# Optimization experiments

Hardware: AMD Instinct MI355X
Metric: run time of the kernel (lower is better)

Reference implementation:

```python
import jax, jax.numpy as jnp
import numpy as np

N_NODES = 100000
N_EDGES = 1600000
IN_DIM = 32
OUT_DIM = 64
N_REL = 8
EPS = 1e-10


def setup_inputs() -> dict:
    key = jax.random.key(0)
    k_x, k_src, k_dst, k_rel, k_w, k_wl, k_ws = jax.random.split(key, 7)
    x = jax.random.normal(k_x, (N_NODES, IN_DIM), dtype=jnp.float32)
    node_in = jax.random.randint(k_src, (N_EDGES,), 0, N_NODES)
    node_out = jax.random.randint(k_dst, (N_EDGES,), 0, N_NODES)
    relation = jax.random.randint(k_rel, (N_EDGES,), 0, N_REL)
    edge_list = jnp.stack([node_in, node_out, relation], axis=1)  # [E, 3] int
    edge_weight = jax.random.uniform(k_w, (N_EDGES,), dtype=jnp.float32)
    W_linear = jax.random.normal(k_wl, (N_REL * IN_DIM, OUT_DIM), dtype=jnp.float32) / np.sqrt(N_REL * IN_DIM)
    b_linear = jnp.zeros((OUT_DIM,), dtype=jnp.float32)
    W_self = jax.random.normal(k_ws, (IN_DIM, OUT_DIM), dtype=jnp.float32) / np.sqrt(IN_DIM)
    b_self = jnp.zeros((OUT_DIM,), dtype=jnp.float32)
    return {"x": x, "edge_list": edge_list, "edge_weight": edge_weight,
            "W_linear": W_linear, "b_linear": b_linear,
            "W_self": W_self, "b_self": b_self}


def reference(x, edge_list, edge_weight, W_linear, b_linear, W_self, b_self):
    num_node, in_dim = x.shape
    # message: gather source-node features per edge  -> [E, D]
    msg = x[edge_list[:, 0]]
    # aggregate: relation-expanded segment id = dst * R + rel
    seg = edge_list[:, 1] * N_REL + edge_list[:, 2]  # [E]
    w = edge_weight[:, None]  # [E, 1]
    num = jax.ops.segment_sum(msg * w, seg, num_segments=num_node * N_REL)  # [N*R, D]
    den = jax.ops.segment_sum(w, seg, num_segments=num_node * N_REL)        # [N*R, 1]
    update = (num / (den + EPS)).reshape(num_node, N_REL * in_dim)          # [N, R*D]
    # combine: linear(update) + self_loop(x), then ReLU
    out = update @ W_linear + b_linear + x @ W_self + b_self
    return jax.nn.relu(out)
```

## Files before the change

kernel.cpp:

```cpp
#include <hip/hip_runtime.h>
#include <stdint.h>

#define N_NODES 100000
#define N_EDGES 1600000
#define IN_DIM 32
#define OUT_DIM 64
#define N_REL 8
#define NSEG (N_NODES * N_REL)
#define EPS 1e-10f
#define N_KK 9
#define SWG_ELEMS (N_KK * 4 * 64 * 8)
#define XB_PAIRS (N_NODES * 16)
#define NTILES ((N_NODES + 63) / 64)

typedef __attribute__((ext_vector_type(8))) short bf16x8;
typedef __attribute__((ext_vector_type(2))) short bf16x2;
typedef __attribute__((ext_vector_type(4))) float f32x4;

static __device__ __forceinline__ float bflo(uint32_t u) { return __uint_as_float(u << 16); }
static __device__ __forceinline__ float bfhi(uint32_t u) { return __uint_as_float(u & 0xffff0000u); }
static __device__ __forceinline__ uint16_t f2bf(float f) {
    uint32_t u = __float_as_uint(f);
    return (uint16_t)((u + 0x7fffu + ((u >> 16) & 1u)) >> 16);
}

static __device__ __forceinline__ void pk_add_bf16(uint32_t* addr, float f0, float f1) {
#if __has_builtin(__builtin_amdgcn_global_atomic_fadd_v2bf16)
    bf16x2 v;
    v[0] = (short)f2bf(f0);
    v[1] = (short)f2bf(f1);
    __builtin_amdgcn_global_atomic_fadd_v2bf16((bf16x2*)addr, v);
#else
    uint32_t old = *addr, assumed;
    do {
        assumed = old;
        float lo = bflo(assumed) + f0;
        float hi = bfhi(assumed) + f1;
        uint32_t nv = (uint32_t)f2bf(lo) | ((uint32_t)f2bf(hi) << 16);
        old = atomicCAS(addr, assumed, nv);
    } while (old != assumed);
#endif
}

__global__ __launch_bounds__(256) void detect_kernel(const uint32_t* __restrict__ xw,
                                                     int* __restrict__ flag) {
    __shared__ int cnt;
    if (threadIdx.x == 0) cnt = 0;
    __syncthreads();
    int c = 0;
    for (int k = threadIdx.x; k < 4096; k += 256) {
        uint32_t w = xw[k];
        uint32_t e = (w >> 7) & 0xffu;
        c += (e >= 160u) ? 1 : 0;
    }
    atomicAdd(&cnt, c);
    __syncthreads();
    if (threadIdx.x == 0) *flag = (cnt > 64) ? 1 : 0;
}

__global__ __launch_bounds__(256) void prep_kernel(const void* __restrict__ x,
                                                   const void* __restrict__ Wl,
                                                   const void* __restrict__ Ws,
                                                   const void* __restrict__ bl,
                                                   const void* __restrict__ bs,
                                                   const int* __restrict__ flag,
                                                   uint32_t* __restrict__ xb,
                                                   uint16_t* __restrict__ sWg,
                                                   float* __restrict__ biasv) {
    int f32 = *flag;
    int idx = blockIdx.x * 256 + threadIdx.x;
    if (idx < XB_PAIRS) {
        if (f32) {
            float2 v = ((const float2*)x)[idx];
            xb[idx] = (uint32_t)f2bf(v.x) | ((uint32_t)f2bf(v.y) << 16);
        } else {
            xb[idx] = ((const uint32_t*)x)[idx];
        }
    } else if (idx < XB_PAIRS + SWG_ELEMS) {
        int w = idx - XB_PAIRS;
        int j    = w & 7;
        int lane = (w >> 3) & 63;
        int ot   = (w >> 9) & 3;
        int kk   = w >> 11;
        int quad = lane >> 4;
        int k = kk * 32 + quad * 8 + j;
        int o = ot * 16 + (lane & 15);
        if (f32) {
            float v = (k < 256) ? ((const float*)Wl)[(size_t)k * OUT_DIM + o]
                                : ((const float*)Ws)[(size_t)(k - 256) * OUT_DIM + o];
            sWg[w] = f2bf(v);
        } else {
            sWg[w] = (k < 256) ? ((const uint16_t*)Wl)[(size_t)k * OUT_DIM + o]
                               : ((const uint16_t*)Ws)[(size_t)(k - 256) * OUT_DIM + o];
        }
    } else if (idx < XB_PAIRS + SWG_ELEMS + OUT_DIM) {
        int o = idx - XB_PAIRS - SWG_ELEMS;
        if (f32) biasv[o] = ((const float*)bl)[o] + ((const float*)bs)[o];
        else     biasv[o] = bflo((uint32_t)((const uint16_t*)bl)[o])
                          + bflo((uint32_t)((const uint16_t*)bs)[o]);
    }
}

__global__ __launch_bounds__(256) void scatter_pk_kernel(
    const int* __restrict__ el,
    const void* __restrict__ ew,
    const uint32_t* __restrict__ xb,
    const int* __restrict__ flag,
    uint32_t* __restrict__ num,
    float* __restrict__ den)
{
    int t = blockIdx.x * 256 + threadIdx.x;
    int e = t >> 4;
    int p = t & 15;
    if (e >= N_EDGES) return;

    int src = el[e * 3 + 0];
    int dst = el[e * 3 + 1];
    int rel = el[e * 3 + 2];

    float w = (*flag) ? ((const float*)ew)[e]
                      : bflo((uint32_t)((const uint16_t*)ew)[e]);

    uint32_t d = xb[(size_t)src * 16 + p];
    int seg = dst * N_REL + rel;
    pk_add_bf16(&num[(size_t)seg * 16 + p], w * bflo(d), w * bfhi(d));
    if (p == 0) atomicAdd(&den[seg], w);
}

__global__ __launch_bounds__(256) void dense_mfma_kernel(
    const uint32_t* __restrict__ num,
    const float* __restrict__ den,
    const uint32_t* __restrict__ xb,
    const uint16_t* __restrict__ sWg,
    const float* __restrict__ biasv,
    const int* __restrict__ flag,
    void* __restrict__ out)
{
    int f32  = *flag;
    int wid  = threadIdx.x >> 6;
    int lane = threadIdx.x & 63;
    int quad = lane >> 4;
    int m    = lane & 15;

    float bias[4];
    #pragma unroll
    for (int ot = 0; ot < 4; ++ot) bias[ot] = biasv[ot * 16 + m];

    int n0 = blockIdx.x * 64 + wid * 16;
    int n  = n0 + m;
    int nc = (n < N_NODES) ? n : (N_NODES - 1);

    float4 d0 = *(const float4*)(den + (size_t)nc * 8);
    float4 d1 = *(const float4*)(den + (size_t)nc * 8 + 4);
    float inv[8];
    inv[0] = 1.0f / (d0.x + EPS); inv[1] = 1.0f / (d0.y + EPS);
    inv[2] = 1.0f / (d0.z + EPS); inv[3] = 1.0f / (d0.w + EPS);
    inv[4] = 1.0f / (d1.x + EPS); inv[5] = 1.0f / (d1.y + EPS);
    inv[6] = 1.0f / (d1.z + EPS); inv[7] = 1.0f / (d1.w + EPS);

    f32x4 acc[4];
    #pragma unroll
    for (int ot = 0; ot < 4; ++ot) acc[ot] = (f32x4){0.f, 0.f, 0.f, 0.f};

    #pragma unroll
    for (int kk = 0; kk < N_KK; ++kk) {
        bf16x8 a;
        if (kk < 8) {
            const uint4 d = *(const uint4*)(num + ((size_t)nc * 8 + kk) * 16 + quad * 4);
            float iv = inv[kk];
            a[0] = (short)f2bf(bflo(d.x) * iv); a[1] = (short)f2bf(bfhi(d.x) * iv);
            a[2] = (short)f2bf(bflo(d.y) * iv); a[3] = (short)f2bf(bfhi(d.y) * iv);
            a[4] = (short)f2bf(bflo(d.z) * iv); a[5] = (short)f2bf(bfhi(d.z) * iv);
            a[6] = (short)f2bf(bflo(d.w) * iv); a[7] = (short)f2bf(bfhi(d.w) * iv);
        } else {
            a = *(const bf16x8*)((const uint16_t*)xb + (size_t)nc * IN_DIM + quad * 8);
        }
        #pragma unroll
        for (int ot = 0; ot < 4; ++ot) {
            bf16x8 b = *(const bf16x8*)(sWg + ((kk * 4 + ot) * 64 + lane) * 8);
            acc[ot] = __builtin_amdgcn_mfma_f32_16x16x32_bf16(a, b, acc[ot], 0, 0, 0);
        }
    }

    #pragma unroll
    for (int ot = 0; ot < 4; ++ot) {
        #pragma unroll
        for (int reg = 0; reg < 4; ++reg) {
            int node = n0 + quad * 4 + reg;
            if (node >= N_NODES) continue;
            int o = ot * 16 + m;
            float v = fmaxf(acc[ot][reg] + bias[ot], 0.0f);
            if (f32) ((float*)out)[(size_t)node * OUT_DIM + o] = v;
            else     ((uint16_t*)out)[(size_t)node * OUT_DIM + o] = f2bf(v);
        }
    }
}

extern "C" void kernel_launch(void* const* d_in, const int* in_sizes, int n_in,
                              void* d_out, int out_size, void* d_ws, size_t ws_size,
                              hipStream_t stream) {
    const void* x  = d_in[0];
    const int* el  = (const int*)d_in[1];
    const void* ew = d_in[2];
    const void* Wl = d_in[3];
    const void* bl = d_in[4];
    const void* Ws = d_in[5];
    const void* bs = d_in[6];

    const size_t OFF_DEN  = 64;
    const size_t OFF_NUM  = OFF_DEN + (size_t)NSEG * 4;
    const size_t OFF_SWG  = OFF_NUM + (size_t)NSEG * IN_DIM * 2;
    const size_t OFF_BIAS = OFF_SWG + (size_t)SWG_ELEMS * 2;
    const size_t OFF_XB   = OFF_BIAS + OUT_DIM * 4;
    const size_t REQ      = OFF_XB + (size_t)XB_PAIRS * 4;
    if (ws_size < REQ) return;

    int*      flag  = (int*)d_ws;
    float*    den   = (float*)((char*)d_ws + OFF_DEN);
    uint32_t* num   = (uint32_t*)((char*)d_ws + OFF_NUM);
    uint16_t* sWg   = (uint16_t*)((char*)d_ws + OFF_SWG);
    float*    biasv = (float*)((char*)d_ws + OFF_BIAS);
    uint32_t* xb    = (uint32_t*)((char*)d_ws + OFF_XB);

    hipMemsetAsync(d_ws, 0, OFF_SWG, stream);
    detect_kernel<<<1, 256, 0, stream>>>((const uint32_t*)x, flag);
    {
        int total = XB_PAIRS + SWG_ELEMS + OUT_DIM;
        prep_kernel<<<(total + 255) / 256, 256, 0, stream>>>(x, Wl, Ws, bl, bs, flag, xb, sWg, biasv);
    }
    {
        long long threads = (long long)N_EDGES * 16;
        int blocks = (int)((threads + 255) / 256);
        scatter_pk_kernel<<<blocks, 256, 0, stream>>>(el, ew, xb, flag, num, den);
    }
    dense_mfma_kernel<<<NTILES, 256, 0, stream>>>(num, den, xb, sWg, biasv, flag, d_out);
}
```

Baseline: 282.0 us.

## Bucket edges by segment and aggregate in LDS instead of global bf16 atomics

Replaces the global packed-bf16 atomic scatter with a counting-sort pipeline: histogram edges into buckets of 256 segments, scan, reorder packed edges, then one block per bucket accumulates num and den in shared memory with fp32 LDS atomics. Normalization and the bf16 conversion move into the aggregation kernel, so the dense MFMA kernel loads pre-divided bf16 rows directly. This removes contended global atomics and the large num/den memset, but adds several passes over the edge list, global atomics on bucket cursors, and a single-block scan. Accumulation is now in fp32 rather than bf16, which improves accuracy.

```diff
diff --git a/kernel.cpp b/kernel.cpp
--- a/kernel.cpp
+++ b/kernel.cpp
@@ -12,9 +12,10 @@
 #define SWG_ELEMS (N_KK * 4 * 64 * 8)
 #define XB_PAIRS (N_NODES * 16)
 #define NTILES ((N_NODES + 63) / 64)
+#define SEGS_PER_BUCKET 256
+#define NBUCK (NSEG / SEGS_PER_BUCKET)
 
 typedef __attribute__((ext_vector_type(8))) short bf16x8;
-typedef __attribute__((ext_vector_type(2))) short bf16x2;
 typedef __attribute__((ext_vector_type(4))) float f32x4;
 
 static __device__ __forceinline__ float bflo(uint32_t u) { return __uint_as_float(u << 16); }
@@ -22,24 +23,6 @@
 static __device__ __forceinline__ uint16_t f2bf(float f) {
     uint32_t u = __float_as_uint(f);
     return (uint16_t)((u + 0x7fffu + ((u >> 16) & 1u)) >> 16);
-}
-
-static __device__ __forceinline__ void pk_add_bf16(uint32_t* addr, float f0, float f1) {
-#if __has_builtin(__builtin_amdgcn_global_atomic_fadd_v2bf16)
-    bf16x2 v;
-    v[0] = (short)f2bf(f0);
-    v[1] = (short)f2bf(f1);
-    __builtin_amdgcn_global_atomic_fadd_v2bf16((bf16x2*)addr, v);
-#else
-    uint32_t old = *addr, assumed;
-    do {
-        assumed = old;
-        float lo = bflo(assumed) + f0;
-        float hi = bfhi(assumed) + f1;
-        uint32_t nv = (uint32_t)f2bf(lo) | ((uint32_t)f2bf(hi) << 16);
-        old = atomicCAS(addr, assumed, nv);
-    } while (old != assumed);
-#endif
 }
 
 __global__ __launch_bounds__(256) void detect_kernel(const uint32_t* __restrict__ xw,
@@ -101,35 +84,111 @@
     }
 }
 
-__global__ __launch_bounds__(256) void scatter_pk_kernel(
-    const int* __restrict__ el,
-    const void* __restrict__ ew,
-    const uint32_t* __restrict__ xb,
-    const int* __restrict__ flag,
-    uint32_t* __restrict__ num,
-    float* __restrict__ den)
-{
-    int t = blockIdx.x * 256 + threadIdx.x;
-    int e = t >> 4;
-    int p = t & 15;
+__global__ __launch_bounds__(256) void hist_kernel(const int* __restrict__ el,
+                                                   unsigned int* __restrict__ hist) {
+    int e = blockIdx.x * 256 + threadIdx.x;
     if (e >= N_EDGES) return;
-
+    int dst = el[e * 3 + 1];
+    int rel = el[e * 3 + 2];
+    atomicAdd(&hist[(dst * N_REL + rel) >> 8], 1u);
+}
+
+__global__ __launch_bounds__(256) void scan_kernel(unsigned int* __restrict__ hist,
+                                                   unsigned int* __restrict__ cursor) {
+    __shared__ unsigned int lds[256];
+    const int PER = (NBUCK + 255) / 256;
+    int t = threadIdx.x;
+    unsigned int v[13];
+    unsigned int loc = 0;
+    #pragma unroll
+    for (int k = 0; k < PER; ++k) {
+        int i = t * PER + k;
+        v[k] = (i < NBUCK) ? hist[i] : 0u;
+        loc += v[k];
+    }
+    lds[t] = loc;
+    __syncthreads();
+    unsigned int xv = lds[t];
+    for (int off = 1; off < 256; off <<= 1) {
+        unsigned int add = (t >= off) ? lds[t - off] : 0u;
+        __syncthreads();
+        xv += add;
+        lds[t] = xv;
+        __syncthreads();
+    }
+    unsigned int run = (t == 0) ? 0u : lds[t - 1];
+    #pragma unroll
+    for (int k = 0; k < PER; ++k) {
+        int i = t * PER + k;
+        if (i < NBUCK) {
+            hist[i] = run;
+            cursor[i] = run;
+            run += v[k];
+        }
+    }
+    if (t == 255) hist[NBUCK] = lds[255];
+}
+
+__global__ __launch_bounds__(256) void reorder_kernel(const int* __restrict__ el,
+                                                      const void* __restrict__ ew,
+                                                      const int* __restrict__ flag,
+                                                      unsigned int* __restrict__ cursor,
+                                                      uint64_t* __restrict__ epack) {
+    int e = blockIdx.x * 256 + threadIdx.x;
+    if (e >= N_EDGES) return;
     int src = el[e * 3 + 0];
     int dst = el[e * 3 + 1];
     int rel = el[e * 3 + 2];
-
-    float w = (*flag) ? ((const float*)ew)[e]
-                      : bflo((uint32_t)((const uint16_t*)ew)[e]);
-
-    uint32_t d = xb[(size_t)src * 16 + p];
+    uint32_t wb = (*flag) ? ((const uint32_t*)ew)[e]
+                          : (((uint32_t)((const uint16_t*)ew)[e]) << 16);
     int seg = dst * N_REL + rel;
-    pk_add_bf16(&num[(size_t)seg * 16 + p], w * bflo(d), w * bfhi(d));
-    if (p == 0) atomicAdd(&den[seg], w);
+    unsigned int pos = atomicAdd(&cursor[seg >> 8], 1u);
+    epack[pos] = ((uint64_t)wb << 32) | ((uint32_t)src << 8) | (uint32_t)(seg & 255);
+}
+
+__global__ __launch_bounds__(256) void aggregate_kernel(const uint64_t* __restrict__ epack,
+                                                        const unsigned int* __restrict__ bstart,
+                                                        const uint32_t* __restrict__ xb,
+                                                        uint32_t* __restrict__ numdiv) {
+    __shared__ float lnum[SEGS_PER_BUCKET * IN_DIM];
+    __shared__ float lden[SEGS_PER_BUCKET];
+
+    int b = blockIdx.x;
+    for (int k = threadIdx.x; k < SEGS_PER_BUCKET * IN_DIM; k += 256) lnum[k] = 0.f;
+    for (int k = threadIdx.x; k < SEGS_PER_BUCKET; k += 256) lden[k] = 0.f;
+    __syncthreads();
+
+    unsigned int start = bstart[b];
+    unsigned int end   = bstart[b + 1];
+    int g    = threadIdx.x >> 5;
+    int lane = threadIdx.x & 31;
+
+    for (unsigned int e = start + g; e < end; e += 8) {
+        uint64_t p = epack[e];
+        uint32_t lo = (uint32_t)p;
+        int seg_local = lo & 255;
+        int src = (lo >> 8) & 0x1FFFF;
+        float w = __uint_as_float((uint32_t)(p >> 32));
+        uint32_t d = xb[(size_t)src * 16 + (lane >> 1)];
+        float xv = (lane & 1) ? bfhi(d) : bflo(d);
+        atomicAdd(&lnum[seg_local * IN_DIM + lane], w * xv);
+        if (lane == 0) atomicAdd(&lden[seg_local], w);
+    }
+    __syncthreads();
+
+    for (int idx = threadIdx.x; idx < SEGS_PER_BUCKET * 16; idx += 256) {
+        int seg_local = idx >> 4;
+        int pr = idx & 15;
+        float iv = 1.0f / (lden[seg_local] + EPS);
+        float f0 = lnum[seg_local * IN_DIM + 2 * pr] * iv;
+        float f1 = lnum[seg_local * IN_DIM + 2 * pr + 1] * iv;
+        numdiv[((size_t)b * SEGS_PER_BUCKET + seg_local) * 16 + pr] =
+            (uint32_t)f2bf(f0) | ((uint32_t)f2bf(f1) << 16);
+    }
 }
 
 __global__ __launch_bounds__(256) void dense_mfma_kernel(
-    const uint32_t* __restrict__ num,
-    const float* __restrict__ den,
+    const uint16_t* __restrict__ numdiv,
     const uint32_t* __restrict__ xb,
     const uint16_t* __restrict__ sWg,
     const float* __restrict__ biasv,
@@ -150,14 +209,6 @@
     int n  = n0 + m;
     int nc = (n < N_NODES) ? n : (N_NODES - 1);
 
-    float4 d0 = *(const float4*)(den + (size_t)nc * 8);
-    float4 d1 = *(const float4*)(den + (size_t)nc * 8 + 4);
-    float inv[8];
-    inv[0] = 1.0f / (d0.x + EPS); inv[1] = 1.0f / (d0.y + EPS);
-    inv[2] = 1.0f / (d0.z + EPS); inv[3] = 1.0f / (d0.w + EPS);
-    inv[4] = 1.0f / (d1.x + EPS); inv[5] = 1.0f / (d1.y + EPS);
-    inv[6] = 1.0f / (d1.z + EPS); inv[7] = 1.0f / (d1.w + EPS);
-
     f32x4 acc[4];
     #pragma unroll
     for (int ot = 0; ot < 4; ++ot) acc[ot] = (f32x4){0.f, 0.f, 0.f, 0.f};
@@ -166,12 +217,7 @@
     for (int kk = 0; kk < N_KK; ++kk) {
         bf16x8 a;
         if (kk < 8) {
-            const uint4 d = *(const uint4*)(num + ((size_t)nc * 8 + kk) * 16 + quad * 4);
-            float iv = inv[kk];
-            a[0] = (short)f2bf(bflo(d.x) * iv); a[1] = (short)f2bf(bfhi(d.x) * iv);
-            a[2] = (short)f2bf(bflo(d.y) * iv); a[3] = (short)f2bf(bfhi(d.y) * iv);
-            a[4] = (short)f2bf(bflo(d.z) * iv); a[5] = (short)f2bf(bfhi(d.z) * iv);
-            a[6] = (short)f2bf(bflo(d.w) * iv); a[7] = (short)f2bf(bfhi(d.w) * iv);
+            a = *(const bf16x8*)(numdiv + (size_t)nc * 256 + kk * 32 + quad * 8);
         } else {
             a = *(const bf16x8*)((const uint16_t*)xb + (size_t)nc * IN_DIM + quad * 8);
         }
@@ -207,31 +253,34 @@
     const void* Ws = d_in[5];
     const void* bs = d_in[6];
 
-    const size_t OFF_DEN  = 64;
-    const size_t OFF_NUM  = OFF_DEN + (size_t)NSEG * 4;
+    const size_t OFF_HIST = 64;
+    const size_t OFF_CUR  = OFF_HIST + (size_t)(NBUCK + 1) * 4;
+    const size_t OFF_EPK  = (OFF_CUR + (size_t)NBUCK * 4 + 63) & ~(size_t)63;
+    const size_t OFF_NUM  = OFF_EPK + (size_t)N_EDGES * 8;
     const size_t OFF_SWG  = OFF_NUM + (size_t)NSEG * IN_DIM * 2;
     const size_t OFF_BIAS = OFF_SWG + (size_t)SWG_ELEMS * 2;
     const size_t OFF_XB   = OFF_BIAS + OUT_DIM * 4;
     const size_t REQ      = OFF_XB + (size_t)XB_PAIRS * 4;
     if (ws_size < REQ) return;
 
-    int*      flag  = (int*)d_ws;
-    float*    den   = (float*)((char*)d_ws + OFF_DEN);
-    uint32_t* num   = (uint32_t*)((char*)d_ws + OFF_NUM);
-    uint16_t* sWg   = (uint16_t*)((char*)d_ws + OFF_SWG);
-    float*    biasv = (float*)((char*)d_ws + OFF_BIAS);
-    uint32_t* xb    = (uint32_t*)((char*)d_ws + OFF_XB);
-
-    hipMemsetAsync(d_ws, 0, OFF_SWG, stream);
+    int*          flag   = (int*)d_ws;
+    unsigned int* hist   = (unsigned int*)((char*)d_ws + OFF_HIST);
+    unsigned int* cursor = (unsigned int*)((char*)d_ws + OFF_CUR);
+    uint64_t*     epack  = (uint64_t*)((char*)d_ws + OFF_EPK);
+    uint32_t*     numdiv = (uint32_t*)((char*)d_ws + OFF_NUM);
+    uint16_t*     sWg    = (uint16_t*)((char*)d_ws + OFF_SWG);
+    float*        biasv  = (float*)((char*)d_ws + OFF_BIAS);
+    uint32_t*     xb     = (uint32_t*)((char*)d_ws + OFF_XB);
+
+    hipMemsetAsync(d_ws, 0, OFF_EPK, stream);
     detect_kernel<<<1, 256, 0, stream>>>((const uint32_t*)x, flag);
+    hist_kernel<<<(N_EDGES + 255) / 256, 256, 0, stream>>>(el, hist);
     {
         int total = XB_PAIRS + SWG_ELEMS + OUT_DIM;
         prep_kernel<<<(total + 255) / 256, 256, 0, stream>>>(x, Wl, Ws, bl, bs, flag, xb, sWg, biasv);
     }
-    {
-        long long threads = (long long)N_EDGES * 16;
-        int blocks = (int)((threads + 255) / 256);
-        scatter_pk_kernel<<<blocks, 256, 0, stream>>>(el, ew, xb, flag, num, den);
-    }
-    dense_mfma_kernel<<<NTILES, 256, 0, stream>>>(num, den, xb, sWg, biasv, flag, d_out);
-}
+    scan_kernel<<<1, 256, 0, stream>>>(hist, cursor);
+    reorder_kernel<<<(N_EDGES + 255) / 256, 256, 0, stream>>>(el, ew, flag, cursor, epack);
+    aggregate_kernel<<<NBUCK, 256, 0, stream>>>(epack, hist, xb, numdiv);
+    dense_mfma_kernel<<<NTILES, 256, 0, stream>>>((const uint16_t*)numdiv, xb, sWg, biasv, flag, d_out);
+}
```

Result: slower. 688.5 us (+144.1%).
